# Performance work log

Measured on AMD Instinct MI355X. Metric: run time of the kernel, lower is better.

The kernel has to match this reference:

```python
import jax, jax.numpy as jnp
import numpy as np

N, E = 50000, 800000
D_IN, H, D_OUT = 100, 128, 40
N_MID = 2  # num_layers(5) - 3
EPS = 1e-5


def setup_inputs() -> dict:
    key = jax.random.key(0)
    ks = iter(jax.random.split(key, 40))
    rn = lambda shape, s=0.05: jax.random.normal(next(ks), shape, dtype=jnp.float32) * s
    inp = {
        "x": jax.random.normal(next(ks), (N, D_IN), dtype=jnp.float32),
        "edge_index": jax.random.randint(next(ks), (2, E), 0, N, dtype=jnp.int64),
        "percent": 70,
        "ricci_curvature": jax.random.normal(next(ks), (E,), dtype=jnp.float32),
        # GCNConv weights/biases
        "W1": rn((D_IN, H)), "b1": jnp.zeros((H,), jnp.float32),
        "W2": rn((D_IN + H, H)), "b2": jnp.zeros((H,), jnp.float32),
        "Wm": rn((N_MID, 2 * H, H)), "bm": jnp.zeros((N_MID, H), jnp.float32),
        "Wo": rn((2 * H, D_OUT)), "bo": jnp.zeros((D_OUT,), jnp.float32),
    }
    # BatchNorm1d params + running stats (eval mode)
    def bn_params(dim, lead=()):
        return (jnp.ones(lead + (dim,), jnp.float32),            # gamma
                jnp.zeros(lead + (dim,), jnp.float32),           # beta
                rn(lead + (dim,), 0.1),                          # running mean
                1.0 + 0.1 * jax.random.uniform(next(ks), lead + (dim,), dtype=jnp.float32))  # running var
    inp["bn1_g"], inp["bn1_b"], inp["bn1_m"], inp["bn1_v"] = bn_params(D_IN)
    inp["bn2_g"], inp["bn2_b"], inp["bn2_m"], inp["bn2_v"] = bn_params(D_IN + H)
    inp["bnm_g"], inp["bnm_b"], inp["bnm_m"], inp["bnm_v"] = bn_params(2 * H, (N_MID,))
    inp["bno_g"], inp["bno_b"], inp["bno_m"], inp["bno_v"] = bn_params(2 * H)
    return inp


def reference(x, edge_index, percent, ricci_curvature,
              W1, b1, W2, b2, Wm, bm, Wo, bo,
              bn1_g, bn1_b, bn1_m, bn1_v,
              bn2_g, bn2_b, bn2_m, bn2_v,
              bnm_g, bnm_b, bnm_m, bnm_v,
              bno_g, bno_b, bno_m, bno_v):
    # Eval mode: no sampling / dynamic edge weights, dropout = identity,
    # BN uses running stats. GCNConv = PyG: add self-loops, sym-norm D^-1/2 A D^-1/2.
    n = x.shape[0]
    loop = jnp.arange(n)
    src = jnp.concatenate([edge_index[0], loop])  # [E+N]
    dst = jnp.concatenate([edge_index[1], loop])
    deg = jnp.zeros((n,), x.dtype).at[dst].add(1.0)  # >=1 thanks to self-loops
    dis = jax.lax.rsqrt(deg)
    norm = (dis[src] * dis[dst])[:, None]  # [E+N, 1]

    def gcn(h, W, b):
        hw = h @ W  # [N, out]
        agg = jnp.zeros((n, W.shape[1]), h.dtype).at[dst].add(hw[src] * norm)
        return agg + b

    def bn(h, g, bta, m, v):
        return (h - m) * (g * jax.lax.rsqrt(v + EPS)) + bta

    res = []
    x_in = x
    h = jax.nn.relu(gcn(bn(x, bn1_g, bn1_b, bn1_m, bn1_v), W1, b1))
    res.append(h)
    h = jnp.concatenate([h, x_in], axis=1)  # [N, H+D_IN]
    h = jax.nn.relu(gcn(bn(h, bn2_g, bn2_b, bn2_m, bn2_v), W2, b2))
    res.append(h)
    h = jnp.concatenate([h, res[-2]], axis=1)  # [N, 2H]
    for i in range(Wm.shape[0]):
        hi = jax.nn.relu(gcn(bn(h, bnm_g[i], bnm_b[i], bnm_m[i], bnm_v[i]), Wm[i], bm[i]))
        res.append(hi)
        h = jnp.concatenate([hi, res[-2]], axis=1)
    out = gcn(bn(h, bno_g, bno_b, bno_m, bno_v), Wo, bo)
    return (out, *res)
```

## Files before the change

### kernel.cpp

```cpp
#include <hip/hip_runtime.h>
#include <hip/hip_bf16.h>
#include <cstdint>
#include <cstddef>

#define BN_EPS 1e-5f
typedef long long ll;
using bf16x8 = __attribute__((ext_vector_type(8))) short;
using f32x4  = __attribute__((ext_vector_type(4))) float;

__device__ __forceinline__ unsigned short f2bf(float f) {
    union { float f; unsigned u; } c; c.f = f;
    unsigned u = c.u;
    u += 0x7fff + ((u >> 16) & 1);
    return (unsigned short)(u >> 16);
}
__device__ __forceinline__ float bf2f(unsigned h) {
    union { unsigned u; float f; } c; c.u = h << 16;
    return c.f;
}
__device__ __forceinline__ void addbf(float* a, uint2 v) {
    a[0] += bf2f(v.x & 0xffffu); a[1] += bf2f(v.x >> 16);
    a[2] += bf2f(v.y & 0xffffu); a[3] += bf2f(v.y >> 16);
}
__device__ __forceinline__ float4 bf4_to_f4(uint2 v) {
    return make_float4(bf2f(v.x & 0xffffu), bf2f(v.x >> 16),
                       bf2f(v.y & 0xffffu), bf2f(v.y >> 16));
}

__global__ void build0_kernel(const int* ei32, int* flag, int* deg, int* cursor, int N) {
    int i = blockIdx.x * 256 + threadIdx.x;
    if (i < N) { deg[i] = 1; cursor[i] = 0; }
    if (blockIdx.x == 0) {
        __shared__ int any;
        if (threadIdx.x == 0) any = 0;
        __syncthreads();
        for (int t = threadIdx.x; t < 2048; t += 256)
            if (ei32[2 * t + 1] != 0) any = 1;
        __syncthreads();
        if (threadIdx.x == 0) *flag = (any == 0) ? 1 : 0;
    }
}

__global__ void count_kernel(const void* ei, int E, int* deg, const int* flag) {
    int e = blockIdx.x * 256 + threadIdx.x;
    if (e >= E) return;
    int d = (*flag) ? (int)((const ll*)ei)[(size_t)E + e]
                    : ((const int*)ei)[(size_t)E + e];
    atomicAdd(&deg[d], 1);
}

__global__ __launch_bounds__(1024) void scanA_kernel(const int* deg, int* row_ptr,
                                                     int* bsum, float* dis, int N) {
    __shared__ int wsum[16];
    int i = blockIdx.x * 1024 + threadIdx.x;
    int lane = threadIdx.x & 63, wid = threadIdx.x >> 6;
    int dv = (i < N) ? deg[i] : 1;
    if (i < N) dis[i] = rsqrtf((float)dv);
    int v = (i < N) ? (dv - 1) : 0;
    int s = v;
#pragma unroll
    for (int o = 1; o < 64; o <<= 1) { int t = __shfl_up(s, o); if (lane >= o) s += t; }
    if (lane == 63) wsum[wid] = s;
    __syncthreads();
    if (threadIdx.x < 16) {
        int w = wsum[threadIdx.x];
        int ws_ = w;
#pragma unroll
        for (int o = 1; o < 16; o <<= 1) { int t = __shfl_up(ws_, o); if ((int)threadIdx.x >= o) ws_ += t; }
        wsum[threadIdx.x] = ws_ - w;
    }
    __syncthreads();
    s += wsum[wid];
    if (i < N) row_ptr[i + 1] = s;
    if (threadIdx.x == 1023) bsum[blockIdx.x] = s;
}

__global__ void scanB_kernel(int* bsum, int nb) {
    int lane = threadIdx.x;
    int v = (lane < nb) ? bsum[lane] : 0;
    int s = v;
#pragma unroll
    for (int o = 1; o < 64; o <<= 1) { int t = __shfl_up(s, o); if (lane >= o) s += t; }
    if (lane < nb) bsum[lane] = s - v;
}

__global__ __launch_bounds__(1024) void scanC_kernel(int* row_ptr, const int* bsum, int N) {
    int i = blockIdx.x * 1024 + threadIdx.x;
    if (i < N) row_ptr[i + 1] += bsum[blockIdx.x];
    if (i == 0) row_ptr[0] = 0;
}

__global__ void fill_kernel(const void* ei, int E, const int* row_ptr,
                            int* cursor, int* csr, const int* flag) {
    int e = blockIdx.x * 256 + threadIdx.x;
    if (e >= E) return;
    int s, d;
    if (*flag) { const ll* p = (const ll*)ei; s = (int)p[e]; d = (int)p[(size_t)E + e]; }
    else       { const int* p = (const int*)ei; s = p[e]; d = p[(size_t)E + e]; }
    int pos = atomicAdd(&cursor[d], 1);
    csr[row_ptr[d] + pos] = s;
}

struct LayerP {
    const float *W, *g, *b, *m, *v;
    int K, Dout, ncb, boff;
};
struct LayerPs { LayerP l[5]; };

__global__ __launch_bounds__(256) void fold_all(LayerPs P,
                                                unsigned short* __restrict__ Bhi,
                                                unsigned short* __restrict__ Blo,
                                                float* __restrict__ cvecA) {
    const LayerP& L = P.l[blockIdx.y];
    if (blockIdx.x < 128) {
        int nkc = (L.K + 63) >> 6 << 1;
        int total = nkc * L.ncb * 512;
        int idx = blockIdx.x * 256 + threadIdx.x;
        if (idx >= total) return;
        int i = idx & 7;
        int lane = (idx >> 3) & 63;
        int cb = (idx >> 9) % L.ncb;
        int kc = (idx >> 9) / L.ncb;
        int k = kc * 32 + (lane >> 4) * 8 + i;
        int col = cb * 16 + (lane & 15);
        float val = 0.f;
        if (k < L.K && col < L.Dout) {
            float s = L.g[k] * rsqrtf(L.v[k] + BN_EPS);
            val = L.W[k * L.Dout + col] * s;
        }
        unsigned short h = f2bf(val);
        Bhi[L.boff + idx] = h;
        Blo[L.boff + idx] = f2bf(val - bf2f(h));
    } else {
        int wid = threadIdx.x >> 6, lane = threadIdx.x & 63;
        int col = (blockIdx.x - 128) * 4 + wid;
        float acc = 0.f;
        if (col < L.Dout) {
            for (int k = lane; k < L.K; k += 64) {
                float s = L.g[k] * rsqrtf(L.v[k] + BN_EPS);
                acc += (L.b[k] - L.m[k] * s) * L.W[k * L.Dout + col];
            }
        }
#pragma unroll
        for (int o = 32; o >= 1; o >>= 1) acc += __shfl_xor(acc, o);
        if (lane == 0 && col < 128) cvecA[128 * blockIdx.y + col] = (col < L.Dout) ? acc : 0.f;
    }
}

__global__ __launch_bounds__(256, 4) void gemm_bf2_kernel(
    const unsigned short* __restrict__ X1, int K1, int ld1,
    const unsigned short* __restrict__ X2, int ld2,
    const unsigned short* __restrict__ Bhi, const unsigned short* __restrict__ Blo,
    const float* __restrict__ cvec, const float* __restrict__ dis,
    unsigned short* __restrict__ outp, int K, int N)
{
    __shared__ unsigned short Xs[64 * 64];
    const int tid = threadIdx.x;
    const int w = tid >> 6, lane = tid & 63;
    const int lr = lane & 15, lg = lane >> 4;
    const int brow = blockIdx.x * 64;
    const int nkt = (K + 63) >> 6;
    const int cb0 = 2 * w;

    f32x4 acc[4][2];
#pragma unroll
    for (int c = 0; c < 2; ++c) {
        float cv = cvec[(cb0 + c) * 16 + lr];
        f32x4 iv = {cv, cv, cv, cv};
#pragma unroll
        for (int rb = 0; rb < 4; ++rb) acc[rb][c] = iv;
    }

    for (int kt = 0; kt < nkt; ++kt) {
        const int k0 = kt * 64;
#pragma unroll
        for (int p = 0; p < 2; ++p) {
            int idx = p * 256 + tid;
            int r = idx >> 3;
            int sl = idx & 7;
            int grow = brow + r;
            int k = k0 + sl * 8;
            uint4 raw = make_uint4(0, 0, 0, 0);
            if (grow < N) {
                if (k < K1)      raw = *(const uint4*)(X1 + (size_t)grow * ld1 + k);
                else if (k < K)  raw = *(const uint4*)(X2 + (size_t)grow * ld2 + (k - K1));
            }
            *(uint4*)((char*)Xs + r * 128 + ((sl * 16) ^ ((r & 7) << 4))) = raw;
        }
        __syncthreads();

#pragma unroll
        for (int ks = 0; ks < 2; ++ks) {
            const int kcg = kt * 2 + ks;
            bf16x8 a[4];
#pragma unroll
            for (int rb = 0; rb < 4; ++rb) {
                int r = rb * 16 + lr;
                a[rb] = *(const bf16x8*)((const char*)Xs + r * 128 +
                                         ((ks * 64 + lg * 16) ^ ((r & 7) << 4)));
            }
            const bf16x8* bh = (const bf16x8*)Bhi + (size_t)kcg * 8 * 64;
            const bf16x8* bl = (const bf16x8*)Blo + (size_t)kcg * 8 * 64;
#pragma unroll
            for (int c = 0; c < 2; ++c) {
                bf16x8 bhf = bh[(cb0 + c) * 64 + lane];
                bf16x8 blf = bl[(cb0 + c) * 64 + lane];
#pragma unroll
                for (int rb = 0; rb < 4; ++rb) {
                    acc[rb][c] = __builtin_amdgcn_mfma_f32_16x16x32_bf16(a[rb], bhf, acc[rb][c], 0, 0, 0);
                    acc[rb][c] = __builtin_amdgcn_mfma_f32_16x16x32_bf16(a[rb], blf, acc[rb][c], 0, 0, 0);
                }
            }
        }
        __syncthreads();
    }

#pragma unroll
    for (int rb = 0; rb < 4; ++rb) {
#pragma unroll
        for (int r = 0; r < 4; ++r) {
            int grow = brow + rb * 16 + lg * 4 + r;
            if (grow >= N) continue;
            float d = dis[grow];
#pragma unroll
            for (int c = 0; c < 2; ++c)
                outp[(size_t)grow * 128 + (cb0 + c) * 16 + lr] = f2bf(d * acc[rb][c][r]);
        }
    }
}

template <bool B1, bool B2>
__global__ __launch_bounds__(256, 3) void gemm_mix2_kernel(
    const void* __restrict__ X1, int K1, int ld1,
    const void* __restrict__ X2, int ld2,
    const unsigned short* __restrict__ Bhi, const unsigned short* __restrict__ Blo,
    const float* __restrict__ cvec, const float* __restrict__ dis,
    unsigned short* __restrict__ outp, int K, int kc_lo, int N)
{
    __shared__ unsigned short Xhi[64 * 64];
    __shared__ unsigned short Xlo[64 * 64];
    const int tid = threadIdx.x;
    const int w = tid >> 6, lane = tid & 63;
    const int lr = lane & 15, lg = lane >> 4;
    const int brow = blockIdx.x * 64;
    const int nkt = (K + 63) >> 6;
    const int cb0 = 2 * w;

    f32x4 acc[4][2];
#pragma unroll
    for (int c = 0; c < 2; ++c) {
        float cv = cvec[(cb0 + c) * 16 + lr];
        f32x4 iv = {cv, cv, cv, cv};
#pragma unroll
        for (int rb = 0; rb < 4; ++rb) acc[rb][c] = iv;
    }

    for (int kt = 0; kt < nkt; ++kt) {
        const int k0 = kt * 64;
        const bool kt_lo = (kt * 2 + 1) >= kc_lo;
#pragma unroll
        for (int p = 0; p < 4; ++p) {
            int fidx = (p * 256 + tid) * 4;
            int r = fidx >> 6;
            int c = fidx & 63;
            int grow = brow + r;
            int k = k0 + c;
            float4 val = make_float4(0.f, 0.f, 0.f, 0.f);
            if (grow < N) {
                if (k < K1) {
                    if (B1) val = bf4_to_f4(*(const uint2*)((const unsigned short*)X1 + (size_t)grow * ld1 + k));
                    else    val = *(const float4*)((const float*)X1 + (size_t)grow * ld1 + k);
                } else if (k < K) {
                    int kk = k - K1;
                    if (B2) val = bf4_to_f4(*(const uint2*)((const unsigned short*)X2 + (size_t)grow * ld2 + kk));
                    else    val = *(const float4*)((const float*)X2 + (size_t)grow * ld2 + kk);
                }
            }
            unsigned short h0 = f2bf(val.x), h1 = f2bf(val.y),
                           h2 = f2bf(val.z), h3 = f2bf(val.w);
            int b8 = c * 2;
            int addr = r * 128 + (((b8 & 0x70) ^ ((r & 7) << 4)) | (b8 & 8));
            *(uint2*)((char*)Xhi + addr) =
                make_uint2((unsigned)h0 | ((unsigned)h1 << 16),
                           (unsigned)h2 | ((unsigned)h3 << 16));
            if (kt_lo) {
                unsigned short l0 = f2bf(val.x - bf2f(h0)), l1 = f2bf(val.y - bf2f(h1)),
                               l2 = f2bf(val.z - bf2f(h2)), l3 = f2bf(val.w - bf2f(h3));
                *(uint2*)((char*)Xlo + addr) =
                    make_uint2((unsigned)l0 | ((unsigned)l1 << 16),
                               (unsigned)l2 | ((unsigned)l3 << 16));
            }
        }
        __syncthreads();

#pragma unroll
        for (int ks = 0; ks < 2; ++ks) {
            const int kcg = kt * 2 + ks;
            const bool need_lo = (kcg >= kc_lo);
            bf16x8 ah[4], al[4];
#pragma unroll
            for (int rb = 0; rb < 4; ++rb) {
                int r = rb * 16 + lr;
                int off = ((ks * 64 + lg * 16) ^ ((r & 7) << 4));
                ah[rb] = *(const bf16x8*)((const char*)Xhi + r * 128 + off);
                if (need_lo) al[rb] = *(const bf16x8*)((const char*)Xlo + r * 128 + off);
            }
            const bf16x8* bh = (const bf16x8*)Bhi + (size_t)kcg * 8 * 64;
            const bf16x8* bl = (const bf16x8*)Blo + (size_t)kcg * 8 * 64;
#pragma unroll
            for (int c = 0; c < 2; ++c) {
                bf16x8 bhf = bh[(cb0 + c) * 64 + lane];
                bf16x8 blf = bl[(cb0 + c) * 64 + lane];
#pragma unroll
                for (int rb = 0; rb < 4; ++rb) {
                    acc[rb][c] = __builtin_amdgcn_mfma_f32_16x16x32_bf16(ah[rb], bhf, acc[rb][c], 0, 0, 0);
                    acc[rb][c] = __builtin_amdgcn_mfma_f32_16x16x32_bf16(ah[rb], blf, acc[rb][c], 0, 0, 0);
                    if (need_lo)
                        acc[rb][c] = __builtin_amdgcn_mfma_f32_16x16x32_bf16(al[rb], bhf, acc[rb][c], 0, 0, 0);
                }
            }
        }
        __syncthreads();
    }

#pragma unroll
    for (int rb = 0; rb < 4; ++rb) {
#pragma unroll
        for (int r = 0; r < 4; ++r) {
            int grow = brow + rb * 16 + lg * 4 + r;
            if (grow >= N) continue;
            float d = dis[grow];
#pragma unroll
            for (int c = 0; c < 2; ++c)
                outp[(size_t)grow * 128 + (cb0 + c) * 16 + lr] = f2bf(d * acc[rb][c][r]);
        }
    }
}

__global__ __launch_bounds__(256, 4) void gemm_bf40_kernel(
    const unsigned short* __restrict__ X1, int K1, int ld1,
    const unsigned short* __restrict__ X2, int ld2,
    const unsigned short* __restrict__ Bhi, const unsigned short* __restrict__ Blo,
    const float* __restrict__ cvec, const float* __restrict__ dis,
    unsigned short* __restrict__ outp, int K, int N)
{
    __shared__ unsigned short Xs[64 * 64];
    const int tid = threadIdx.x;
    const int w = tid >> 6, lane = tid & 63;
    const int lr = lane & 15, lg = lane >> 4;
    const int brow = blockIdx.x * 64;
    const int nkt = (K + 63) >> 6;

    f32x4 acc[3];
#pragma unroll
    for (int cb = 0; cb < 3; ++cb) {
        float cv = cvec[cb * 16 + lr];
        f32x4 iv = {cv, cv, cv, cv};
        acc[cb] = iv;
    }

    for (int kt = 0; kt < nkt; ++kt) {
        const int k0 = kt * 64;
#pragma unroll
        for (int p = 0; p < 2; ++p) {
            int idx = p * 256 + tid;
            int r = idx >> 3;
            int sl = idx & 7;
            int grow = brow + r;
            int k = k0 + sl * 8;
            uint4 raw = make_uint4(0, 0, 0, 0);
            if (grow < N) {
                if (k < K1)      raw = *(const uint4*)(X1 + (size_t)grow * ld1 + k);
                else if (k < K)  raw = *(const uint4*)(X2 + (size_t)grow * ld2 + (k - K1));
            }
            *(uint4*)((char*)Xs + r * 128 + ((sl * 16) ^ ((r & 7) << 4))) = raw;
        }
        __syncthreads();

        const int r = w * 16 + lr;
        const char* base = (const char*)Xs + r * 128;
        const int swz = (r & 7) << 4;
        bf16x8 a0 = *(const bf16x8*)(base + ((lg * 16) ^ swz));
        bf16x8 a1 = *(const bf16x8*)(base + ((64 + lg * 16) ^ swz));
#pragma unroll
        for (int ks = 0; ks < 2; ++ks) {
            const int kcg = kt * 2 + ks;
            const bf16x8 af = ks ? a1 : a0;
            const bf16x8* bh = (const bf16x8*)Bhi + (size_t)kcg * 3 * 64;
            const bf16x8* bl = (const bf16x8*)Blo + (size_t)kcg * 3 * 64;
#pragma unroll
            for (int cb = 0; cb < 3; ++cb) {
                bf16x8 bhf = bh[cb * 64 + lane];
                bf16x8 blf = bl[cb * 64 + lane];
                acc[cb] = __builtin_amdgcn_mfma_f32_16x16x32_bf16(af, bhf, acc[cb], 0, 0, 0);
                acc[cb] = __builtin_amdgcn_mfma_f32_16x16x32_bf16(af, blf, acc[cb], 0, 0, 0);
            }
        }
        __syncthreads();
    }

#pragma unroll
    for (int r = 0; r < 4; ++r) {
        int grow = brow + w * 16 + lg * 4 + r;
        if (grow >= N) continue;
        float d = dis[grow];
#pragma unroll
        for (int cb = 0; cb < 3; ++cb) {
            int col = cb * 16 + lr;
            if (col < 40) outp[(size_t)grow * 40 + col] = f2bf(d * acc[cb][r]);
        }
    }
}

template <bool RELU>
__global__ __launch_bounds__(256) void agg128b_kernel(
    const unsigned short* __restrict__ hwb,
    const int* __restrict__ row_ptr, const int* __restrict__ csr,
    const float* __restrict__ dis, const float* __restrict__ bias,
    float* __restrict__ outp, unsigned short* __restrict__ hbout, int N)
{
    int wid = threadIdx.x >> 6, lane = threadIdx.x & 63;
    int node = blockIdx.x * 4 + wid;
    if (node >= N) return;
    const int half = lane >> 5, q = lane & 31;
    const uint2* hw2 = (const uint2*)hwb;
    float a[4] = {0.f, 0.f, 0.f, 0.f};
    float b4[4] = {0.f, 0.f, 0.f, 0.f};
    if (half == 0) addbf(a, hw2[(size_t)node * 32 + q]);
    int beg = row_ptr[node], end = row_ptr[node + 1];
    for (int base = beg; base < end; base += 64) {
        int idx = base + lane;
        int j = (idx < end) ? csr[idx] : 0;
        int cnt = end - base; if (cnt > 64) cnt = 64;
        int fullp = cnt >> 1;
        int t = 0;
        for (; t + 4 <= fullp; t += 4) {
            int ja = __shfl(j, 2 * t     + half);
            int jb = __shfl(j, 2 * t + 2 + half);
            int jc = __shfl(j, 2 * t + 4 + half);
            int jd = __shfl(j, 2 * t + 6 + half);
            uint2 va = hw2[(size_t)ja * 32 + q];
            uint2 vb = hw2[(size_t)jb * 32 + q];
            uint2 vc = hw2[(size_t)jc * 32 + q];
            uint2 vd = hw2[(size_t)jd * 32 + q];
            addbf(a, va); addbf(b4, vb); addbf(a, vc); addbf(b4, vd);
        }
        for (; t < fullp; ++t) {
            int ja = __shfl(j, 2 * t + half);
            uint2 va = hw2[(size_t)ja * 32 + q];
            addbf(a, va);
        }
        if (cnt & 1) {
            int ja = __shfl(j, cnt - 1);
            if (half == 0) { uint2 va = hw2[(size_t)ja * 32 + q]; addbf(a, va); }
        }
    }
#pragma unroll
    for (int c = 0; c < 4; ++c) {
        a[c] += b4[c];
        a[c] += __shfl_xor(a[c], 32);
    }
    if (half == 0) {
        float d = dis[node];
        float4 bv = ((const float4*)bias)[q];
        float4 o;
        o.x = fmaf(d, a[0], bv.x);
        o.y = fmaf(d, a[1], bv.y);
        o.z = fmaf(d, a[2], bv.z);
        o.w = fmaf(d, a[3], bv.w);
        if (RELU) {
            o.x = fmaxf(o.x, 0.f); o.y = fmaxf(o.y, 0.f);
            o.z = fmaxf(o.z, 0.f); o.w = fmaxf(o.w, 0.f);
        }
        ((float4*)outp)[(size_t)node * 32 + q] = o;
        uint2 pk;
        pk.x = (unsigned)f2bf(o.x) | ((unsigned)f2bf(o.y) << 16);
        pk.y = (unsigned)f2bf(o.z) | ((unsigned)f2bf(o.w) << 16);
        ((uint2*)hbout)[(size_t)node * 32 + q] = pk;
    }
}

__global__ __launch_bounds__(256) void agg40b_kernel(
    const unsigned short* __restrict__ hwb,
    const int* __restrict__ row_ptr, const int* __restrict__ csr,
    const float* __restrict__ dis, const float* __restrict__ bias,
    float* __restrict__ outp, int N)
{
    int wid = threadIdx.x >> 6, lane = threadIdx.x & 63;
    int node = blockIdx.x * 4 + wid;
    if (node >= N) return;
    const int half = lane >> 5, q = lane & 31;
    const bool act = q < 20;
    const unsigned* hw20 = (const unsigned*)hwb;
    float a0 = 0.f, a1 = 0.f, b0 = 0.f, b1 = 0.f;
    if (half == 0 && act) {
        unsigned v = hw20[(size_t)node * 20 + q];
        a0 += bf2f(v & 0xffffu); a1 += bf2f(v >> 16);
    }
    int beg = row_ptr[node], end = row_ptr[node + 1];
    for (int base = beg; base < end; base += 64) {
        int idx = base + lane;
        int j = (idx < end) ? csr[idx] : 0;
        int cnt = end - base; if (cnt > 64) cnt = 64;
        int fullp = cnt >> 1;
        int t = 0;
        for (; t + 4 <= fullp; t += 4) {
            int ja = __shfl(j, 2 * t     + half);
            int jb = __shfl(j, 2 * t + 2 + half);
            int jc = __shfl(j, 2 * t + 4 + half);
            int jd = __shfl(j, 2 * t + 6 + half);
            if (act) {
                unsigned va = hw20[(size_t)ja * 20 + q];
                unsigned vb = hw20[(size_t)jb * 20 + q];
                unsigned vc = hw20[(size_t)jc * 20 + q];
                unsigned vd = hw20[(size_t)jd * 20 + q];
                a0 += bf2f(va & 0xffffu); a1 += bf2f(va >> 16);
                b0 += bf2f(vb & 0xffffu); b1 += bf2f(vb >> 16);
                a0 += bf2f(vc & 0xffffu); a1 += bf2f(vc >> 16);
                b0 += bf2f(vd & 0xffffu); b1 += bf2f(vd >> 16);
            }
        }
        for (; t < fullp; ++t) {
            int ja = __shfl(j, 2 * t + half);
            if (act) {
                unsigned va = hw20[(size_t)ja * 20 + q];
                a0 += bf2f(va & 0xffffu); a1 += bf2f(va >> 16);
            }
        }
        if (cnt & 1) {
            int ja = __shfl(j, cnt - 1);
            if (half == 0 && act) {
                unsigned va = hw20[(size_t)ja * 20 + q];
                a0 += bf2f(va & 0xffffu); a1 += bf2f(va >> 16);
            }
        }
    }
    a0 += b0; a1 += b1;
    a0 += __shfl_xor(a0, 32);
    a1 += __shfl_xor(a1, 32);
    if (half == 0 && act) {
        float d = dis[node];
        float2 o;
        o.x = fmaf(d, a0, bias[2 * q]);
        o.y = fmaf(d, a1, bias[2 * q + 1]);
        *(float2*)(outp + (size_t)node * 40 + 2 * q) = o;
    }
}

extern "C" void kernel_launch(void* const* d_in, const int* in_sizes, int n_in,
                              void* d_out, int out_size, void* d_ws, size_t ws_size,
                              hipStream_t stream) {
    const int N = in_sizes[0] / 100;
    const int E = in_sizes[1] / 2;

    const float* x   = (const float*)d_in[0];
    const void*  ei  = d_in[1];
    const float* W1  = (const float*)d_in[4];
    const float* b1  = (const float*)d_in[5];
    const float* W2  = (const float*)d_in[6];
    const float* b2  = (const float*)d_in[7];
    const float* Wm  = (const float*)d_in[8];
    const float* bm  = (const float*)d_in[9];
    const float* Wo  = (const float*)d_in[10];
    const float* bo  = (const float*)d_in[11];
    const float* bn1g = (const float*)d_in[12];
    const float* bn1b = (const float*)d_in[13];
    const float* bn1m = (const float*)d_in[14];
    const float* bn1v = (const float*)d_in[15];
    const float* bn2g = (const float*)d_in[16];
    const float* bn2b = (const float*)d_in[17];
    const float* bn2m = (const float*)d_in[18];
    const float* bn2v = (const float*)d_in[19];
    const float* bnmg = (const float*)d_in[20];
    const float* bnmb = (const float*)d_in[21];
    const float* bnmm = (const float*)d_in[22];
    const float* bnmv = (const float*)d_in[23];
    const float* bnog = (const float*)d_in[24];
    const float* bnob = (const float*)d_in[25];
    const float* bnom = (const float*)d_in[26];
    const float* bnov = (const float*)d_in[27];

    char* wsb = (char*)d_ws;
    size_t off = 0;
    auto alloc = [&](size_t elems) -> void* { void* p = wsb + off; off += elems * 4; return p; };
    int*   deg     = (int*)alloc(N);
    int*   cursor  = (int*)alloc(N);
    int*   row_ptr = (int*)alloc((size_t)N + 1);
    int*   bsum    = (int*)alloc(64);
    int*   flag    = (int*)alloc(1);
    off = (off + 15) & ~(size_t)15;
    float* dis  = (float*)alloc(N);
    int*   csr  = (int*)alloc(E);
    off = (off + 15) & ~(size_t)15;
    unsigned short* hwb = (unsigned short*)alloc((size_t)N * 64);
    unsigned short* hbA = (unsigned short*)alloc((size_t)N * 64);
    unsigned short* hbB = (unsigned short*)alloc((size_t)N * 64);
    unsigned short* hbC = (unsigned short*)alloc((size_t)N * 64);
    unsigned short* BhiA = (unsigned short*)alloc(63488);
    unsigned short* BloA = (unsigned short*)alloc(63488);
    float* cvecA = (float*)alloc(128 * 5);
    (void)ws_size; (void)n_in; (void)out_size;

    float* outF = (float*)d_out;
    float* h1 = outF + (size_t)N * 40;
    float* h2 = h1 + (size_t)N * 128;
    float* h3 = h2 + (size_t)N * 128;
    float* h4 = h3 + (size_t)N * 128;

    dim3 b256(256);

    LayerPs P;
    P.l[0] = {W1, bn1g, bn1b, bn1m, bn1v, 100, 128, 8, 0};
    P.l[1] = {W2, bn2g, bn2b, bn2m, bn2v, 228, 128, 8, 16384};
    P.l[2] = {Wm, bnmg, bnmb, bnmm, bnmv, 256, 128, 8, 49152};
    P.l[3] = {Wm + 256 * 128, bnmg + 256, bnmb + 256, bnmm + 256, bnmv + 256, 256, 128, 8, 81920};
    P.l[4] = {Wo, bnog, bnob, bnom, bnov, 256, 40, 3, 114688};
    fold_all<<<dim3(160, 5), b256, 0, stream>>>(P, BhiA, BloA, cvecA);

    build0_kernel<<<dim3((N + 255) / 256), b256, 0, stream>>>((const int*)ei, flag, deg, cursor, N);
    count_kernel<<<dim3((E + 255) / 256), b256, 0, stream>>>(ei, E, deg, flag);
    int nb = (N + 1023) / 1024;
    scanA_kernel<<<dim3(nb), dim3(1024), 0, stream>>>(deg, row_ptr, bsum, dis, N);
    scanB_kernel<<<1, 64, 0, stream>>>(bsum, nb);
    scanC_kernel<<<dim3(nb), dim3(1024), 0, stream>>>(row_ptr, bsum, N);
    fill_kernel<<<dim3((E + 255) / 256), b256, 0, stream>>>(ei, E, row_ptr, cursor, csr, flag);

    int gemm_grid = (N + 63) / 64;
    int agg_grid  = (N + 3) / 4;

    auto agg128 = [&](const float* lb, float* dst, unsigned short* hbout) {
        agg128b_kernel<true><<<dim3(agg_grid), b256, 0, stream>>>(
            hwb, row_ptr, csr, dis, lb, dst, hbout, N);
    };

    gemm_mix2_kernel<false, false><<<dim3(gemm_grid), b256, 0, stream>>>(
        x, 100, 100, nullptr, 0, BhiA + P.l[0].boff, BloA + P.l[0].boff,
        cvecA, dis, hwb, 100, 0, N);
    agg128(b1, h1, hbA);

    gemm_mix2_kernel<true, false><<<dim3(gemm_grid), b256, 0, stream>>>(
        hbA, 128, 128, x, 100, BhiA + P.l[1].boff, BloA + P.l[1].boff,
        cvecA + 128, dis, hwb, 228, 4, N);
    agg128(b2, h2, hbB);

    gemm_bf2_kernel<<<dim3(gemm_grid), b256, 0, stream>>>(
        hbB, 128, 128, hbA, 128, BhiA + P.l[2].boff, BloA + P.l[2].boff,
        cvecA + 256, dis, hwb, 256, N);
    agg128(bm, h3, hbC);

    gemm_bf2_kernel<<<dim3(gemm_grid), b256, 0, stream>>>(
        hbC, 128, 128, hbB, 128, BhiA + P.l[3].boff, BloA + P.l[3].boff,
        cvecA + 384, dis, hwb, 256, N);
    agg128(bm + 128, h4, hbA);

    gemm_bf40_kernel<<<dim3(gemm_grid), b256, 0, stream>>>(
        hbA, 128, 128, hbC, 128, BhiA + P.l[4].boff, BloA + P.l[4].boff,
        cvecA + 512, dis, hwb, 256, N);
    agg40b_kernel<<<dim3(agg_grid), b256, 0, stream>>>(hwb, row_ptr, csr, dis, bo, outF, N);
}
```

Measured before the change: 382.7 us.

## Split 128-wide GCN aggregation into eight column slices across blocks

The 128-column aggregation kernel now launches eight times as many blocks. Each block covers one 16-column slice for four nodes, and each wave gathers 16 neighbors at once with 4 lanes per neighbor. A wider shuffle reduction across lane groups then merges the partial sums. The goal is more memory-level parallelism and more waves in flight for the irregular neighbor gather. The cost is that the CSR indices and row pointers are re-read once per slice, and each gather touches only a 32-byte piece of a row, which may lower cache-line efficiency.

```diff
diff --git a/kernel.cpp b/kernel.cpp
--- a/kernel.cpp
+++ b/kernel.cpp
@@ -18,7 +18,7 @@
     union { unsigned u; float f; } c; c.u = h << 16;
     return c.f;
 }
-__device__ __forceinline__ void addbf(float* a, uint2 v) {
+__device__ __forceinline__ void addbf4(float* a, uint2 v) {
     a[0] += bf2f(v.x & 0xffffu); a[1] += bf2f(v.x >> 16);
     a[2] += bf2f(v.y & 0xffffu); a[3] += bf2f(v.y >> 16);
 }
@@ -413,56 +413,63 @@
 }
 
 template <bool RELU>
-__global__ __launch_bounds__(256) void agg128b_kernel(
+__global__ __launch_bounds__(256) void agg128s_kernel(
     const unsigned short* __restrict__ hwb,
     const int* __restrict__ row_ptr, const int* __restrict__ csr,
     const float* __restrict__ dis, const float* __restrict__ bias,
     float* __restrict__ outp, unsigned short* __restrict__ hbout, int N)
 {
     int wid = threadIdx.x >> 6, lane = threadIdx.x & 63;
-    int node = blockIdx.x * 4 + wid;
+    int slice = blockIdx.x & 7;
+    int node = (blockIdx.x >> 3) * 4 + wid;
     if (node >= N) return;
-    const int half = lane >> 5, q = lane & 31;
+    const int g = lane >> 2, u = lane & 3;
     const uint2* hw2 = (const uint2*)hwb;
+    const int soff = slice * 4 + u;
     float a[4] = {0.f, 0.f, 0.f, 0.f};
     float b4[4] = {0.f, 0.f, 0.f, 0.f};
-    if (half == 0) addbf(a, hw2[(size_t)node * 32 + q]);
+    if (g == 0) addbf4(a, hw2[(size_t)node * 32 + soff]);
     int beg = row_ptr[node], end = row_ptr[node + 1];
     for (int base = beg; base < end; base += 64) {
         int idx = base + lane;
         int j = (idx < end) ? csr[idx] : 0;
         int cnt = end - base; if (cnt > 64) cnt = 64;
-        int fullp = cnt >> 1;
+        int fullg = cnt >> 4;
         int t = 0;
-        for (; t + 4 <= fullp; t += 4) {
-            int ja = __shfl(j, 2 * t     + half);
-            int jb = __shfl(j, 2 * t + 2 + half);
-            int jc = __shfl(j, 2 * t + 4 + half);
-            int jd = __shfl(j, 2 * t + 6 + half);
-            uint2 va = hw2[(size_t)ja * 32 + q];
-            uint2 vb = hw2[(size_t)jb * 32 + q];
-            uint2 vc = hw2[(size_t)jc * 32 + q];
-            uint2 vd = hw2[(size_t)jd * 32 + q];
-            addbf(a, va); addbf(b4, vb); addbf(a, vc); addbf(b4, vd);
-        }
-        for (; t < fullp; ++t) {
-            int ja = __shfl(j, 2 * t + half);
-            uint2 va = hw2[(size_t)ja * 32 + q];
-            addbf(a, va);
-        }
-        if (cnt & 1) {
-            int ja = __shfl(j, cnt - 1);
-            if (half == 0) { uint2 va = hw2[(size_t)ja * 32 + q]; addbf(a, va); }
+        for (; t + 2 <= fullg; t += 2) {
+            int ja = __shfl(j, 16 * t + g);
+            int jb = __shfl(j, 16 * t + 16 + g);
+            uint2 va = hw2[(size_t)ja * 32 + soff];
+            uint2 vb = hw2[(size_t)jb * 32 + soff];
+            addbf4(a, va); addbf4(b4, vb);
+        }
+        for (; t < fullg; ++t) {
+            int ja = __shfl(j, 16 * t + g);
+            uint2 va = hw2[(size_t)ja * 32 + soff];
+            addbf4(a, va);
+        }
+        int rem = cnt & 15;
+        if (rem) {
+            int srcl = (cnt & ~15) + ((g < rem) ? g : 0);
+            int ja = __shfl(j, srcl);
+            if (g < rem) {
+                uint2 va = hw2[(size_t)ja * 32 + soff];
+                addbf4(a, va);
+            }
         }
     }
 #pragma unroll
     for (int c = 0; c < 4; ++c) {
         a[c] += b4[c];
+        a[c] += __shfl_xor(a[c], 4);
+        a[c] += __shfl_xor(a[c], 8);
+        a[c] += __shfl_xor(a[c], 16);
         a[c] += __shfl_xor(a[c], 32);
     }
-    if (half == 0) {
+    if (g == 0) {
         float d = dis[node];
-        float4 bv = ((const float4*)bias)[q];
+        int col0 = slice * 16 + u * 4;
+        float4 bv = *(const float4*)(bias + col0);
         float4 o;
         o.x = fmaf(d, a[0], bv.x);
         o.y = fmaf(d, a[1], bv.y);
@@ -472,11 +479,11 @@
             o.x = fmaxf(o.x, 0.f); o.y = fmaxf(o.y, 0.f);
             o.z = fmaxf(o.z, 0.f); o.w = fmaxf(o.w, 0.f);
         }
-        ((float4*)outp)[(size_t)node * 32 + q] = o;
+        *(float4*)(outp + (size_t)node * 128 + col0) = o;
         uint2 pk;
         pk.x = (unsigned)f2bf(o.x) | ((unsigned)f2bf(o.y) << 16);
         pk.y = (unsigned)f2bf(o.z) | ((unsigned)f2bf(o.w) << 16);
-        ((uint2*)hbout)[(size_t)node * 32 + q] = pk;
+        *(uint2*)(hbout + (size_t)node * 128 + col0) = pk;
     }
 }
 
@@ -626,10 +633,11 @@
     fill_kernel<<<dim3((E + 255) / 256), b256, 0, stream>>>(ei, E, row_ptr, cursor, csr, flag);
 
     int gemm_grid = (N + 63) / 64;
+    int aggs_grid = ((N + 3) / 4) * 8;
     int agg_grid  = (N + 3) / 4;
 
     auto agg128 = [&](const float* lb, float* dst, unsigned short* hbout) {
-        agg128b_kernel<true><<<dim3(agg_grid), b256, 0, stream>>>(
+        agg128s_kernel<true><<<dim3(aggs_grid), b256, 0, stream>>>(
             hwb, row_ptr, csr, dis, lb, dst, hbout, N);
     };
 
```

After: 835.1 us. 118% more time.
